# Kernel optimization log

Measured on AMD Instinct MI355X. Metric: run time of the kernel, lower is better.

## Reference

```python
import jax, jax.numpy as jnp
import numpy as np

B, S, E, H = 2, 2048, 1024, 16
D = E // H  # head_size = 64


def setup_inputs() -> dict:
    key = jax.random.key(0)
    ks = jax.random.split(key, 11)
    sc = 0.02
    return {
        "q": jax.random.normal(ks[0], (B, S, E), jnp.float32),
        "k": jax.random.normal(ks[1], (B, S, E), jnp.float32),
        "v": jax.random.normal(ks[2], (B, S, E), jnp.float32),
        "Wq": jax.random.normal(ks[3], (E, E), jnp.float32) * sc,
        "bq": jnp.zeros((E,), jnp.float32),
        "Wk": jax.random.normal(ks[4], (E, E), jnp.float32) * sc,
        "bk": jnp.zeros((E,), jnp.float32),
        "Wv": jax.random.normal(ks[5], (E, E), jnp.float32) * sc,
        "bv": jnp.zeros((E,), jnp.float32),
        "Wo": jax.random.normal(ks[6], (E, E), jnp.float32) * sc,
        "bo": jnp.zeros((E,), jnp.float32),
    }


def reference(q, k, v, Wq, bq, Wk, bk, Wv, bv, Wo, bo):
    # torch Linear: y = x @ W.T + b
    qh = (q @ Wq.T + bq).reshape(B, S, H, D)
    kh = (k @ Wk.T + bk).reshape(B, S, H, D)
    vh = (v @ Wv.T + bv).reshape(B, S, H, D)
    # NOTE: module scales by 1/sqrt(num_heads), not 1/sqrt(head_size)
    scores = jnp.einsum('bqhe,bkhe->bhqk', qh, kh) / jnp.sqrt(jnp.float32(H))
    attn = jax.nn.softmax(scores, axis=-1)  # dropout is identity in eval
    out = jnp.einsum('bhql,blhd->bqhd', attn, vh)  # [B,S,H,D]
    out = out.reshape(B, S, E)
    return out @ Wo.T + bo
```

## Files before the change

### kernel.cpp

```cpp
#include <hip/hip_runtime.h>

typedef __bf16 bf16x8 __attribute__((ext_vector_type(8)));
typedef __bf16 bf16x4 __attribute__((ext_vector_type(4)));
typedef float  f32x4  __attribute__((ext_vector_type(4)));
typedef short  s16x4  __attribute__((ext_vector_type(4)));

#define AS1 __attribute__((address_space(1)))
#define AS3 __attribute__((address_space(3)))

__device__ inline void gload_lds16(const void* g, void* l) {
  __builtin_amdgcn_global_load_lds((AS1 void*)(g), (AS3 void*)(l), 16, 0, 0);
}

#if __has_builtin(__builtin_amdgcn_exp2f)
#define EXP2(x) __builtin_amdgcn_exp2f(x)
#else
#define EXP2(x) exp2f(x)
#endif

#if __has_builtin(__builtin_amdgcn_mfma_f32_16x16x16bf16_1k)
#define PV_K16 1
#define MFMA16(a, b, c) __builtin_amdgcn_mfma_f32_16x16x16bf16_1k(a, b, c, 0, 0, 0)
#else
#define PV_K16 0
#endif

__device__ inline short bf2s(__bf16 x) {
  union { __bf16 b; short s; } u; u.b = x; return u.s;
}

#define CB 2
#define CS 2048
#define CE 1024
#define CH 16
#define CD 64
#define GM 4096
#define GN 1024
#define GK 1024

#define QSCALE 0.36067376022224087f

#define WS_WQ  0
#define WS_WK  1048576
#define WS_WV  2097152
#define WS_WO  3145728
#define WS_XQ  4194304
#define WS_XK  8388608
#define WS_XV  12582912
#define WS_QH  16777216
#define WS_KH  20971520
#define WS_VT  25165824
#define WS_AO  WS_XQ

__global__ __launch_bounds__(256) void convert_all(
    const float* __restrict__ q, const float* __restrict__ k, const float* __restrict__ v,
    const float* __restrict__ wq, const float* __restrict__ wk,
    const float* __restrict__ wv, const float* __restrict__ wo,
    __bf16* __restrict__ ws) {
  long idx = ((long)blockIdx.x * 256 + threadIdx.x) * 8;
  const float* src;
  __bf16* dst;
  if (idx < 12582912) {
    int a = (int)(idx >> 22);
    long within = idx & 4194303;
    src = (a == 0 ? q : (a == 1 ? k : v)) + within;
    dst = ws + WS_XQ + (long)a * 4194304 + within;
  } else {
    long widx = idx - 12582912;
    int a = (int)(widx >> 20);
    long within = widx & 1048575;
    src = (a == 0 ? wq : (a == 1 ? wk : (a == 2 ? wv : wo))) + within;
    dst = ws + widx;
  }
  float4 f0 = *(const float4*)src;
  float4 f1 = *(const float4*)(src + 4);
  bf16x8 o;
  o[0] = (__bf16)f0.x; o[1] = (__bf16)f0.y; o[2] = (__bf16)f0.z; o[3] = (__bf16)f0.w;
  o[4] = (__bf16)f1.x; o[5] = (__bf16)f1.y; o[6] = (__bf16)f1.z; o[7] = (__bf16)f1.w;
  *(bf16x8*)dst = o;
}

__global__ __launch_bounds__(256) void qkv_gemm(
    const __bf16* __restrict__ Xq, const __bf16* __restrict__ Xk, const __bf16* __restrict__ Xv,
    const __bf16* __restrict__ Wq, const __bf16* __restrict__ Wk, const __bf16* __restrict__ Wv,
    const float* __restrict__ bq, const float* __restrict__ bk, const float* __restrict__ bv,
    __bf16* __restrict__ Qh, __bf16* __restrict__ Kh, __bf16* __restrict__ Vt) {
  __shared__ __bf16 As[4096];
  __shared__ __bf16 Bs[8192];
  const int tid = threadIdx.x;
  const int w = tid >> 6, l = tid & 63;
  const int orig = blockIdx.y * gridDim.x + blockIdx.x;
  const int cpx = (gridDim.x * gridDim.y) >> 3;
  const int wgid = (orig & 7) * cpx + (orig >> 3);
  const int bm = (wgid / gridDim.x) * 64, bn = (wgid % gridDim.x) * 128;
  const int lr = l & 15, lq = l >> 4;
  const int srow = w * 8 + (l >> 3);
  const int scol = ((l & 7) ^ ((l >> 3) & 7)) * 8;
  const int dstg = w * 64 + l;

  for (int mode = 0; mode < 3; mode++) {
    const __bf16* A  = mode == 0 ? Xq : (mode == 1 ? Xk : Xv);
    const __bf16* Bw = mode == 0 ? Wq : (mode == 1 ? Wk : Wv);
    const float* bias = mode == 0 ? bq : (mode == 1 ? bk : bv);
    const __bf16* ga0 = A  + (size_t)(bm + srow) * GK + scol;
    const __bf16* gb0 = Bw + (size_t)(bn + srow) * GK + scol;

    f32x4 acc[4][2] = {};
    for (int k0 = 0; k0 < GK; k0 += 64) {
      __syncthreads();
      for (int i = 0; i < 2; i++)
        gload_lds16(ga0 + (size_t)(i * 32) * GK + k0, &As[(i * 256 + dstg) * 8]);
      for (int i = 0; i < 4; i++)
        gload_lds16(gb0 + (size_t)(i * 32) * GK + k0, &Bs[(i * 256 + dstg) * 8]);
      __syncthreads();
      for (int kk = 0; kk < 2; kk++) {
        bf16x8 af[4], bfr[2];
        for (int mi = 0; mi < 4; mi++) {
          const int row = mi * 16 + lr;
          af[mi] = *(const bf16x8*)&As[(row * 8 + ((kk * 4 + lq) ^ (row & 7))) * 8];
        }
        for (int ni = 0; ni < 2; ni++) {
          const int row = w * 32 + ni * 16 + lr;
          bfr[ni] = *(const bf16x8*)&Bs[(row * 8 + ((kk * 4 + lq) ^ (row & 7))) * 8];
        }
        for (int mi = 0; mi < 4; mi++)
          for (int ni = 0; ni < 2; ni++)
            acc[mi][ni] = __builtin_amdgcn_mfma_f32_16x16x32_bf16(af[mi], bfr[ni],
                                                                  acc[mi][ni], 0, 0, 0);
      }
    }

    for (int ni = 0; ni < 2; ni++) {
      const int col = bn + w * 32 + ni * 16 + lr;
      const float bb = bias[col];
      for (int mi = 0; mi < 4; mi++) {
        const int row = bm + mi * 16 + lq * 4;
        if (mode == 0) {
          for (int r = 0; r < 4; r++)
            Qh[(size_t)(row + r) * GN + col] = (__bf16)((acc[mi][ni][r] + bb) * QSCALE);
        } else if (mode == 1) {
          for (int r = 0; r < 4; r++)
            Kh[(size_t)(row + r) * GN + col] = (__bf16)(acc[mi][ni][r] + bb);
        } else {
          const int b = row >> 11, s = row & 2047;
          const int h = col >> 6, d = col & 63;
          bf16x4 pk;
          for (int r = 0; r < 4; r++) pk[r] = (__bf16)(acc[mi][ni][r] + bb);
          *(bf16x4*)&Vt[(size_t)((b * CH + h) * CD + d) * CS + s] = pk;
        }
      }
    }
  }
}

__global__ __launch_bounds__(256) void gemm_wo(const __bf16* __restrict__ Ain,
                                               const __bf16* __restrict__ Bw,
                                               const float* __restrict__ bias,
                                               float* __restrict__ O) {
  __shared__ __bf16 As[4096];
  __shared__ __bf16 Bs[8192];
  const int tid = threadIdx.x;
  const int w = tid >> 6, l = tid & 63;
  const int orig = blockIdx.y * gridDim.x + blockIdx.x;
  const int cpx = (gridDim.x * gridDim.y) >> 3;
  const int wgid = (orig & 7) * cpx + (orig >> 3);
  const int bm = (wgid / gridDim.x) * 64, bn = (wgid % gridDim.x) * 128;
  const int lr = l & 15, lq = l >> 4;
  f32x4 acc[4][2] = {};
  const int srow = w * 8 + (l >> 3);
  const int scol = ((l & 7) ^ ((l >> 3) & 7)) * 8;
  const __bf16* ga0 = Ain + (size_t)(bm + srow) * GK + scol;
  const __bf16* gb0 = Bw + (size_t)(bn + srow) * GK + scol;
  const int dstg = w * 64 + l;
  for (int k0 = 0; k0 < GK; k0 += 64) {
    __syncthreads();
    for (int i = 0; i < 2; i++)
      gload_lds16(ga0 + (size_t)(i * 32) * GK + k0, &As[(i * 256 + dstg) * 8]);
    for (int i = 0; i < 4; i++)
      gload_lds16(gb0 + (size_t)(i * 32) * GK + k0, &Bs[(i * 256 + dstg) * 8]);
    __syncthreads();
    for (int kk = 0; kk < 2; kk++) {
      bf16x8 af[4], bfr[2];
      for (int mi = 0; mi < 4; mi++) {
        const int row = mi * 16 + lr;
        af[mi] = *(const bf16x8*)&As[(row * 8 + ((kk * 4 + lq) ^ (row & 7))) * 8];
      }
      for (int ni = 0; ni < 2; ni++) {
        const int row = w * 32 + ni * 16 + lr;
        bfr[ni] = *(const bf16x8*)&Bs[(row * 8 + ((kk * 4 + lq) ^ (row & 7))) * 8];
      }
      for (int mi = 0; mi < 4; mi++)
        for (int ni = 0; ni < 2; ni++)
          acc[mi][ni] = __builtin_amdgcn_mfma_f32_16x16x32_bf16(af[mi], bfr[ni],
                                                                acc[mi][ni], 0, 0, 0);
    }
  }

  for (int ni = 0; ni < 2; ni++) {
    const int col = bn + w * 32 + ni * 16 + lr;
    const float bb = bias[col];
    for (int mi = 0; mi < 4; mi++) {
      const int row = bm + mi * 16 + lq * 4;
      for (int r = 0; r < 4; r++)
        O[(size_t)(row + r) * GN + col] = acc[mi][ni][r] + bb;
    }
  }
}

__global__ __launch_bounds__(256, 2) void attn(const __bf16* __restrict__ Qh,
                                               const __bf16* __restrict__ Kh,
                                               const __bf16* __restrict__ Vt,
                                               __bf16* __restrict__ AO) {
  __shared__ __bf16 Ks[8192];
  __shared__ __bf16 Vs[8192];

  const int tid = threadIdx.x, w = tid >> 6, l = tid & 63;
  const int lr = l & 15, lq = l >> 4;
  const int bh = blockIdx.x;
  const int b = bh >> 4, h = bh & 15;
  const int q0 = blockIdx.y * 128 + w * 32;

  bf16x8 qf[2][2];
  for (int mi = 0; mi < 2; mi++)
    for (int kk = 0; kk < 2; kk++)
      qf[mi][kk] = *(const bf16x8*)&Qh[((size_t)b * CS + q0 + mi * 16 + lr) * CE + h * CD + kk * 32 + lq * 8];

  f32x4 o[2][4] = {};
  float lsum[2] = {0.f, 0.f};
#if !PV_K16
  const bool hi_half = (lq & 1);
#endif

  for (int kt = 0; kt < CS / 128; kt++) {
    __syncthreads();
    for (int i = 0; i < 4; i++) {
      const int j = w * 2 + (i >> 1), hf = i & 1;
      const int key = (hf * 64 + l) ^ ((j & 3) * 2);
      gload_lds16(&Kh[((size_t)b * CS + kt * 128 + key) * CE + h * CD + j * 8],
                  &Ks[(j * 128 + hf * 64) * 8]);
    }
    for (int i = 0; i < 4; i++) {
      const int j2 = w * 4 + i;
      const int d = l ^ ((j2 & 1) * 4);
      gload_lds16(&Vt[((size_t)bh * CD + d) * CS + kt * 128 + j2 * 8],
                  &Vs[(j2 * 64) * 8]);
    }
    __syncthreads();

    f32x4 sa[2][8] = {};
    for (int kk = 0; kk < 2; kk++) {
      bf16x8 kf[8];
      for (int ni = 0; ni < 8; ni++)
        kf[ni] = *(const bf16x8*)&Ks[((kk * 4 + lq) * 128 + ((ni * 16 + lr) ^ (lq * 2))) * 8];
      for (int mi = 0; mi < 2; mi++)
        for (int ni = 0; ni < 8; ni++)
          sa[mi][ni] = __builtin_amdgcn_mfma_f32_16x16x32_bf16(kf[ni], qf[mi][kk], sa[mi][ni], 0, 0, 0);
    }

#if PV_K16
    for (int ni = 0; ni < 8; ni++) {
      s16x4 pa4[2];
      for (int mi = 0; mi < 2; mi++)
        for (int r = 0; r < 4; r++) {
          const float p = EXP2(sa[mi][ni][r]);
          lsum[mi] += p;
          pa4[mi][r] = bf2s((__bf16)p);
        }
      const int j2 = ni * 2 + (lq >> 1);
      const int base = j2 * 64;
      const int sw = (j2 & 1) * 4;
      for (int di = 0; di < 4; di++) {
        const int dslot = (di * 16 + lr) ^ sw;
        const s16x4 vb4 = *(const s16x4*)&Vs[(base + dslot) * 8 + (lq & 1) * 4];
        for (int mi = 0; mi < 2; mi++)
          o[mi][di] = MFMA16(pa4[mi], vb4, o[mi][di]);
      }
    }
#else
    for (int ni = 0; ni < 8; ni++) {
      bf16x8 pa[2];
      for (int mi = 0; mi < 2; mi++) {
        bf16x8 f;
        for (int r = 0; r < 4; r++) {
          const float p = EXP2(sa[mi][ni][r]);
          lsum[mi] += p;
          const __bf16 bv2 = (__bf16)p;
          f[r]     = hi_half ? (__bf16)0.f : bv2;
          f[4 + r] = hi_half ? bv2 : (__bf16)0.f;
        }
        pa[mi] = f;
      }
      for (int di = 0; di < 4; di++) {
        const bf16x8 vbf = *(const bf16x8*)&Vs[((ni * 2 + (lq >> 1)) * 64 + ((di * 16 + lr) ^ ((lq >> 1) * 4))) * 8];
        for (int mi = 0; mi < 2; mi++)
          o[mi][di] = __builtin_amdgcn_mfma_f32_16x16x32_bf16(pa[mi], vbf, o[mi][di], 0, 0, 0);
      }
    }
#endif
  }

  for (int mi = 0; mi < 2; mi++) {
    lsum[mi] += __shfl_xor(lsum[mi], 16, 64);
    lsum[mi] += __shfl_xor(lsum[mi], 32, 64);
  }

  for (int mi = 0; mi < 2; mi++) {
    f32x4 rv;
    for (int r = 0; r < 4; r++) rv[r] = 1.0f / __shfl(lsum[mi], lq * 4 + r, 64);
    for (int di = 0; di < 4; di++)
      for (int r = 0; r < 4; r++) {
        const size_t s = q0 + mi * 16 + lq * 4 + r;
        AO[((size_t)b * CS + s) * CE + h * CD + di * 16 + lr] = (__bf16)(o[mi][di][r] * rv[r]);
      }
  }
}

extern "C" void kernel_launch(void* const* d_in, const int* in_sizes, int n_in,
                              void* d_out, int out_size, void* d_ws, size_t ws_size,
                              hipStream_t stream) {
  (void)in_sizes; (void)n_in; (void)out_size; (void)ws_size;
  const float* q  = (const float*)d_in[0];
  const float* k  = (const float*)d_in[1];
  const float* v  = (const float*)d_in[2];
  const float* Wq = (const float*)d_in[3];
  const float* bq = (const float*)d_in[4];
  const float* Wk = (const float*)d_in[5];
  const float* bk = (const float*)d_in[6];
  const float* Wv = (const float*)d_in[7];
  const float* bv = (const float*)d_in[8];
  const float* Wo = (const float*)d_in[9];
  const float* bo = (const float*)d_in[10];

  __bf16* ws = (__bf16*)d_ws;
  __bf16 *Wq_b = ws + WS_WQ, *Wk_b = ws + WS_WK, *Wv_b = ws + WS_WV, *Wo_b = ws + WS_WO;
  __bf16 *Xq = ws + WS_XQ, *Xk = ws + WS_XK, *Xv = ws + WS_XV;
  __bf16 *Qh = ws + WS_QH, *Kh = ws + WS_KH, *Vt = ws + WS_VT;
  __bf16 *AO = ws + WS_AO;

  convert_all<<<8192, 256, 0, stream>>>(q, k, v, Wq, Wk, Wv, Wo, ws);

  qkv_gemm<<<dim3(8, 64), 256, 0, stream>>>(
      Xq, Xk, Xv, Wq_b, Wk_b, Wv_b, bq, bk, bv, Qh, Kh, Vt);

  attn<<<dim3(CB * CH, CS / 128), 256, 0, stream>>>(Qh, Kh, Vt, AO);

  gemm_wo<<<dim3(GN / 128, GM / 64), 256, 0, stream>>>(AO, Wo_b, bo, (float*)d_out);
}
```

Measured before the change: 223.7 us.

## Fuse fp32-to-bf16 activation conversion into QKV GEMM and enlarge tiles

The separate conversion pass over the q/k/v activations is dropped. The QKV GEMM now loads fp32 activations directly and converts them to bf16 in registers before storing to LDS, which removes a full write and re-read of 12M bf16 elements. The GEMM is restructured to 128x128 tiles with a 2x2 wave layout and a grid z-dimension over Q/K/V, replacing the serial loop over the three modes. Attention blocks are also remapped across batch-heads to spread them over XCDs. The trade-off is that A-tile loads now go through registers with synchronous conversion instead of async global-to-LDS copies.

```diff
diff --git a/kernel.cpp b/kernel.cpp
--- a/kernel.cpp
+++ b/kernel.cpp
@@ -44,34 +44,20 @@
 #define WS_WK  1048576
 #define WS_WV  2097152
 #define WS_WO  3145728
-#define WS_XQ  4194304
-#define WS_XK  8388608
-#define WS_XV  12582912
 #define WS_QH  16777216
 #define WS_KH  20971520
 #define WS_VT  25165824
-#define WS_AO  WS_XQ
-
-__global__ __launch_bounds__(256) void convert_all(
-    const float* __restrict__ q, const float* __restrict__ k, const float* __restrict__ v,
+#define WS_AO  4194304
+
+__global__ __launch_bounds__(256) void convert_w(
     const float* __restrict__ wq, const float* __restrict__ wk,
     const float* __restrict__ wv, const float* __restrict__ wo,
     __bf16* __restrict__ ws) {
-  long idx = ((long)blockIdx.x * 256 + threadIdx.x) * 8;
-  const float* src;
-  __bf16* dst;
-  if (idx < 12582912) {
-    int a = (int)(idx >> 22);
-    long within = idx & 4194303;
-    src = (a == 0 ? q : (a == 1 ? k : v)) + within;
-    dst = ws + WS_XQ + (long)a * 4194304 + within;
-  } else {
-    long widx = idx - 12582912;
-    int a = (int)(widx >> 20);
-    long within = widx & 1048575;
-    src = (a == 0 ? wq : (a == 1 ? wk : (a == 2 ? wv : wo))) + within;
-    dst = ws + widx;
-  }
+  long widx = ((long)blockIdx.x * 256 + threadIdx.x) * 8;
+  int a = (int)(widx >> 20);
+  long within = widx & 1048575;
+  const float* src = (a == 0 ? wq : (a == 1 ? wk : (a == 2 ? wv : wo))) + within;
+  __bf16* dst = ws + widx;
   float4 f0 = *(const float4*)src;
   float4 f1 = *(const float4*)(src + 4);
   bf16x8 o;
@@ -80,74 +66,87 @@
   *(bf16x8*)dst = o;
 }
 
-__global__ __launch_bounds__(256) void qkv_gemm(
-    const __bf16* __restrict__ Xq, const __bf16* __restrict__ Xk, const __bf16* __restrict__ Xv,
+__global__ __launch_bounds__(256, 3) void qkv_gemm(
+    const float* __restrict__ Aq, const float* __restrict__ Ak, const float* __restrict__ Av,
     const __bf16* __restrict__ Wq, const __bf16* __restrict__ Wk, const __bf16* __restrict__ Wv,
     const float* __restrict__ bq, const float* __restrict__ bk, const float* __restrict__ bv,
     __bf16* __restrict__ Qh, __bf16* __restrict__ Kh, __bf16* __restrict__ Vt) {
-  __shared__ __bf16 As[4096];
+  const int mode = blockIdx.z;
+  const float* A   = mode == 0 ? Aq : (mode == 1 ? Ak : Av);
+  const __bf16* Bw = mode == 0 ? Wq : (mode == 1 ? Wk : Wv);
+  const float* bias = mode == 0 ? bq : (mode == 1 ? bk : bv);
+
+  __shared__ __bf16 As[8192];
   __shared__ __bf16 Bs[8192];
   const int tid = threadIdx.x;
   const int w = tid >> 6, l = tid & 63;
+  const int wm = w >> 1, wn = w & 1;
   const int orig = blockIdx.y * gridDim.x + blockIdx.x;
   const int cpx = (gridDim.x * gridDim.y) >> 3;
   const int wgid = (orig & 7) * cpx + (orig >> 3);
-  const int bm = (wgid / gridDim.x) * 64, bn = (wgid % gridDim.x) * 128;
+  const int bm = (wgid / gridDim.x) * 128, bn = (wgid % gridDim.x) * 128;
   const int lr = l & 15, lq = l >> 4;
+  f32x4 acc[4][4] = {};
   const int srow = w * 8 + (l >> 3);
   const int scol = ((l & 7) ^ ((l >> 3) & 7)) * 8;
+  const float*  ga0 = A  + (size_t)(bm + srow) * GK + scol;
+  const __bf16* gb0 = Bw + (size_t)(bn + srow) * GK + scol;
   const int dstg = w * 64 + l;
 
-  for (int mode = 0; mode < 3; mode++) {
-    const __bf16* A  = mode == 0 ? Xq : (mode == 1 ? Xk : Xv);
-    const __bf16* Bw = mode == 0 ? Wq : (mode == 1 ? Wk : Wv);
-    const float* bias = mode == 0 ? bq : (mode == 1 ? bk : bv);
-    const __bf16* ga0 = A  + (size_t)(bm + srow) * GK + scol;
-    const __bf16* gb0 = Bw + (size_t)(bn + srow) * GK + scol;
-
-    f32x4 acc[4][2] = {};
-    for (int k0 = 0; k0 < GK; k0 += 64) {
-      __syncthreads();
-      for (int i = 0; i < 2; i++)
-        gload_lds16(ga0 + (size_t)(i * 32) * GK + k0, &As[(i * 256 + dstg) * 8]);
-      for (int i = 0; i < 4; i++)
-        gload_lds16(gb0 + (size_t)(i * 32) * GK + k0, &Bs[(i * 256 + dstg) * 8]);
-      __syncthreads();
-      for (int kk = 0; kk < 2; kk++) {
-        bf16x8 af[4], bfr[2];
-        for (int mi = 0; mi < 4; mi++) {
-          const int row = mi * 16 + lr;
-          af[mi] = *(const bf16x8*)&As[(row * 8 + ((kk * 4 + lq) ^ (row & 7))) * 8];
-        }
-        for (int ni = 0; ni < 2; ni++) {
-          const int row = w * 32 + ni * 16 + lr;
-          bfr[ni] = *(const bf16x8*)&Bs[(row * 8 + ((kk * 4 + lq) ^ (row & 7))) * 8];
-        }
-        for (int mi = 0; mi < 4; mi++)
-          for (int ni = 0; ni < 2; ni++)
-            acc[mi][ni] = __builtin_amdgcn_mfma_f32_16x16x32_bf16(af[mi], bfr[ni],
-                                                                  acc[mi][ni], 0, 0, 0);
-      }
-    }
-
-    for (int ni = 0; ni < 2; ni++) {
-      const int col = bn + w * 32 + ni * 16 + lr;
-      const float bb = bias[col];
+  for (int k0 = 0; k0 < GK; k0 += 64) {
+    float4 a0[4], a1[4];
+    for (int i = 0; i < 4; i++) {
+      const float* src = ga0 + (size_t)(i * 32) * GK + k0;
+      a0[i] = *(const float4*)src;
+      a1[i] = *(const float4*)(src + 4);
+    }
+    __syncthreads();
+    for (int i = 0; i < 4; i++) {
+      bf16x8 o8;
+      o8[0] = (__bf16)a0[i].x; o8[1] = (__bf16)a0[i].y;
+      o8[2] = (__bf16)a0[i].z; o8[3] = (__bf16)a0[i].w;
+      o8[4] = (__bf16)a1[i].x; o8[5] = (__bf16)a1[i].y;
+      o8[6] = (__bf16)a1[i].z; o8[7] = (__bf16)a1[i].w;
+      *(bf16x8*)&As[(i * 256 + dstg) * 8] = o8;
+      gload_lds16(gb0 + (size_t)(i * 32) * GK + k0, &Bs[(i * 256 + dstg) * 8]);
+    }
+    __syncthreads();
+    for (int kk = 0; kk < 2; kk++) {
+      bf16x8 af[4], bfr[4];
       for (int mi = 0; mi < 4; mi++) {
-        const int row = bm + mi * 16 + lq * 4;
-        if (mode == 0) {
-          for (int r = 0; r < 4; r++)
-            Qh[(size_t)(row + r) * GN + col] = (__bf16)((acc[mi][ni][r] + bb) * QSCALE);
-        } else if (mode == 1) {
-          for (int r = 0; r < 4; r++)
-            Kh[(size_t)(row + r) * GN + col] = (__bf16)(acc[mi][ni][r] + bb);
-        } else {
-          const int b = row >> 11, s = row & 2047;
-          const int h = col >> 6, d = col & 63;
-          bf16x4 pk;
-          for (int r = 0; r < 4; r++) pk[r] = (__bf16)(acc[mi][ni][r] + bb);
-          *(bf16x4*)&Vt[(size_t)((b * CH + h) * CD + d) * CS + s] = pk;
-        }
+        const int row = wm * 64 + mi * 16 + lr;
+        af[mi] = *(const bf16x8*)&As[(row * 8 + ((kk * 4 + lq) ^ (row & 7))) * 8];
+      }
+      for (int ni = 0; ni < 4; ni++) {
+        const int row = wn * 64 + ni * 16 + lr;
+        bfr[ni] = *(const bf16x8*)&Bs[(row * 8 + ((kk * 4 + lq) ^ (row & 7))) * 8];
+      }
+      for (int mi = 0; mi < 4; mi++)
+        for (int ni = 0; ni < 4; ni++)
+          acc[mi][ni] = __builtin_amdgcn_mfma_f32_16x16x32_bf16(af[mi], bfr[ni],
+                                                                acc[mi][ni], 0, 0, 0);
+    }
+  }
+
+  const int row0 = bm + wm * 64;
+  const int col0 = bn + wn * 64;
+  for (int ni = 0; ni < 4; ni++) {
+    const int col = col0 + ni * 16 + lr;
+    const float bb = bias[col];
+    for (int mi = 0; mi < 4; mi++) {
+      const int row = row0 + mi * 16 + lq * 4;
+      if (mode == 0) {
+        for (int r = 0; r < 4; r++)
+          Qh[(size_t)(row + r) * GN + col] = (__bf16)((acc[mi][ni][r] + bb) * QSCALE);
+      } else if (mode == 1) {
+        for (int r = 0; r < 4; r++)
+          Kh[(size_t)(row + r) * GN + col] = (__bf16)(acc[mi][ni][r] + bb);
+      } else {
+        const int b = row >> 11, s = row & 2047;
+        const int h = col >> 6, d = col & 63;
+        bf16x4 pk;
+        for (int r = 0; r < 4; r++) pk[r] = (__bf16)(acc[mi][ni][r] + bb);
+        *(bf16x4*)&Vt[(size_t)((b * CH + h) * CD + d) * CS + s] = pk;
       }
     }
   }
@@ -216,7 +215,8 @@
 
   const int tid = threadIdx.x, w = tid >> 6, l = tid & 63;
   const int lr = l & 15, lq = l >> 4;
-  const int bh = blockIdx.x;
+  const int bx = blockIdx.x;
+  const int bh = (bx & 7) * 4 + (bx >> 3);
   const int b = bh >> 4, h = bh & 15;
   const int q0 = blockIdx.y * 128 + w * 32;
 
@@ -333,14 +333,13 @@
 
   __bf16* ws = (__bf16*)d_ws;
   __bf16 *Wq_b = ws + WS_WQ, *Wk_b = ws + WS_WK, *Wv_b = ws + WS_WV, *Wo_b = ws + WS_WO;
-  __bf16 *Xq = ws + WS_XQ, *Xk = ws + WS_XK, *Xv = ws + WS_XV;
   __bf16 *Qh = ws + WS_QH, *Kh = ws + WS_KH, *Vt = ws + WS_VT;
   __bf16 *AO = ws + WS_AO;
 
-  convert_all<<<8192, 256, 0, stream>>>(q, k, v, Wq, Wk, Wv, Wo, ws);
-
-  qkv_gemm<<<dim3(8, 64), 256, 0, stream>>>(
-      Xq, Xk, Xv, Wq_b, Wk_b, Wv_b, bq, bk, bv, Qh, Kh, Vt);
+  convert_w<<<2048, 256, 0, stream>>>(Wq, Wk, Wv, Wo, ws);
+
+  qkv_gemm<<<dim3(GN / 128, GM / 128, 3), 256, 0, stream>>>(
+      q, k, v, Wq_b, Wk_b, Wv_b, bq, bk, bv, Qh, Kh, Vt);
 
   attn<<<dim3(CB * CH, CS / 128), 256, 0, stream>>>(Qh, Kh, Vt, AO);
 
```

New measurement: 221.4 us. No clear change (-1.0%).
